# Optimization experiments

Hardware: AMD Instinct MI355X
Metric: run time of the kernel (lower is better)

## Reference

```python
import jax, jax.numpy as jnp
import numpy as np

B, N, H = 8, 512, 256
D2 = H // 2          # per-direction hidden = attention proj = 128
VOCAB, EMB = 100, 256
DIN0 = EMB + 3


def _sru_pp_layer(x, pad, Wq, Wk, Wv, Wu, vf, vr, bf, br):
    # x: (L, Bt, din); pad: (L, Bt) bool, True = padded position
    L, Bt, _ = x.shape
    d2 = Wu.shape[1] // 8
    q = x @ Wq                                   # (L,Bt,proj) attention projection
    k = q @ Wk
    v = q @ Wv
    scale = 1.0 / jnp.sqrt(jnp.asarray(q.shape[-1], q.dtype))
    scores = jnp.einsum('lbp,mbp->blm', q, k) * scale
    scores = jnp.where(pad.T[:, None, :], -1e9, scores)
    a = jnp.einsum('blm,mbp->lbp', jax.nn.softmax(scores, axis=-1), v) + q
    U = (a @ Wu).reshape(L, Bt, 2, 4, d2)        # 2 directions x 4 matrices

    def run_dir(Ud, padd, vf_d, vr_d, bf_d, br_d):
        def step(c, inp):
            u, p = inp                            # u: (Bt,4,d2), p: (Bt,)
            f = jax.nn.sigmoid(u[:, 1] + vf_d * c + bf_d)
            r = jax.nn.sigmoid(u[:, 2] + vr_d * c + br_d)
            c_new = f * c + (1.0 - f) * u[:, 0]
            c_new = jnp.where(p[:, None], c, c_new)
            h = jnp.where(p[:, None], 0.0, r * c_new + (1.0 - r) * u[:, 3])
            return c_new, h
        c0 = jnp.zeros((Bt, d2), x.dtype)
        _, hs = jax.lax.scan(step, c0, (Ud, padd))
        return hs

    hf = run_dir(U[:, :, 0], pad, vf[0], vr[0], bf[0], br[0])
    hb = run_dir(U[::-1, :, 1], pad[::-1], vf[1], vr[1], bf[1], br[1])[::-1]
    return jnp.concatenate([hf, hb], axis=-1)     # (L,Bt,2*d2)


def _forward(noisy_seqs, noisy_cords, mask, emb, params):
    Bb, Nn = noisy_seqs.shape
    X = noisy_cords[:, :, 1]                      # CA coordinates (B,N,3)
    m3 = mask[..., None]
    center = (X * m3).sum(1) / m3.sum(1)
    Xc = X - center[:, None] * m3
    C = jnp.einsum('bni,bnj->bij', Xc, Xc)        # (B,3,3) covariance
    _, V = jnp.linalg.eigh(jax.lax.stop_gradient(C))
    ops = jnp.asarray([[i, j, k] for i in (-1, 1) for j in (-1, 1) for k in (-1, 1)], X.dtype)
    F_ops = ops[None, :, None, :] * V[:, None]    # (B,8,3,3) sign-flipped frames
    hX = jnp.einsum('boji,bpj->bopi', F_ops, Xc).reshape(Bb * 8, Nn, 3)
    seq = jnp.where(noisy_seqs < 0, 82, noisy_seqs)
    hS = jnp.broadcast_to(emb[seq][:, None], (Bb, 8, Nn, emb.shape[1])).reshape(Bb * 8, Nn, -1)
    h = jnp.swapaxes(jnp.concatenate([hX, hS], -1), 0, 1)   # (N, B*8, EMB+3)
    pad = jnp.broadcast_to((mask == 0.0)[:, None], (Bb, 8, Nn)).reshape(Bb * 8, Nn).T
    for p in params:
        h = _sru_pp_layer(h, pad, *p)
    return jnp.swapaxes(h, 0, 1).reshape(Bb, 8, Nn, -1).mean(1)


def setup_inputs():
    key = jax.random.key(0)
    ks = [jax.random.fold_in(key, i) for i in range(32)]
    inp = {
        'noisy_seqs': jax.random.randint(ks[0], (B, N), 0, VOCAB, dtype=jnp.int32),
        'noisy_cords': jax.random.normal(ks[1], (B, N, 4, 3), jnp.float32),
        'mask': jnp.ones((B, N), jnp.float32),
        'emb': 0.02 * jax.random.normal(ks[2], (VOCAB, EMB), jnp.float32),
    }
    i = 3
    for l, din in enumerate([DIN0, H]):
        inp[f'Wq{l}'] = jax.random.normal(ks[i], (din, D2), jnp.float32) / np.sqrt(din); i += 1
        inp[f'Wk{l}'] = jax.random.normal(ks[i], (D2, D2), jnp.float32) / np.sqrt(D2); i += 1
        inp[f'Wv{l}'] = jax.random.normal(ks[i], (D2, D2), jnp.float32) / np.sqrt(D2); i += 1
        inp[f'Wu{l}'] = jax.random.normal(ks[i], (D2, 8 * D2), jnp.float32) / np.sqrt(D2); i += 1
        inp[f'vf{l}'] = 0.1 * jax.random.normal(ks[i], (2, D2), jnp.float32); i += 1
        inp[f'vr{l}'] = 0.1 * jax.random.normal(ks[i], (2, D2), jnp.float32); i += 1
        inp[f'bf{l}'] = jnp.zeros((2, D2), jnp.float32)
        inp[f'br{l}'] = jnp.zeros((2, D2), jnp.float32)
    return inp


def reference(noisy_seqs, noisy_cords, mask, emb,
              Wq0, Wk0, Wv0, Wu0, vf0, vr0, bf0, br0,
              Wq1, Wk1, Wv1, Wu1, vf1, vr1, bf1, br1):
    params = [(Wq0, Wk0, Wv0, Wu0, vf0, vr0, bf0, br0),
              (Wq1, Wk1, Wv1, Wu1, vf1, vr1, bf1, br1)]
    return _forward(noisy_seqs, noisy_cords, mask, emb, params)
```

## Files before the change

kernel.cpp:

```cpp
#include <hip/hip_runtime.h>
#include <hip/hip_bf16.h>
#include <math.h>

#define L_    512
#define F_    64
#define M_    (F_*L_)
#define D2_   128
#define H_    256
#define LOG2E_ 1.4426950408889634f

typedef unsigned short u16;
typedef __attribute__((ext_vector_type(8))) short s16x8;
typedef __attribute__((ext_vector_type(4))) float f32x4;

__device__ inline u16 bf_hi(float x) {
  union { float f; unsigned u; } v; v.f = x;
  unsigned r = v.u + 0x7fffu + ((v.u >> 16) & 1u);
  return (u16)(r >> 16);
}
__device__ inline float bf_to_f(u16 h) {
  union { float f; unsigned u; } v; v.u = ((unsigned)h) << 16; return v.f;
}
__device__ inline void split2(float x, u16& h, u16& l) {
  h = bf_hi(x);
  l = bf_hi(x - bf_to_f(h));
}
__device__ inline float exp2_fast(float x) {
#if __has_builtin(__builtin_amdgcn_exp2f)
  return __builtin_amdgcn_exp2f(x);
#else
  return __expf(x * 0.6931471805599453f);
#endif
}

#define RSPLIT_A 18432
#define RSPLIT_B 26624

__global__ void geom_kernel(const float* __restrict__ cords, const float* __restrict__ mask,
                            float* __restrict__ misc) {
  int b = blockIdx.x;
  int t = threadIdx.x;
  __shared__ float red[4][256];
  float sx=0.f, sy=0.f, sz=0.f, sm=0.f;
  for (int l = t; l < 512; l += 256) {
    float m = mask[b*512 + l];
    const float* X = cords + ((size_t)(b*512 + l)*4 + 1)*3;
    sx += X[0]*m; sy += X[1]*m; sz += X[2]*m; sm += m;
  }
  red[0][t]=sx; red[1][t]=sy; red[2][t]=sz; red[3][t]=sm;
  __syncthreads();
  for (int off=128; off>0; off>>=1) {
    if (t < off) { red[0][t]+=red[0][t+off]; red[1][t]+=red[1][t+off];
                   red[2][t]+=red[2][t+off]; red[3][t]+=red[3][t+off]; }
    __syncthreads();
  }
  float inv = 1.f/red[3][0];
  float cx = red[0][0]*inv, cy = red[1][0]*inv, cz = red[2][0]*inv;
  __syncthreads();
  __shared__ float red6[6][256];
  float c00=0,c01=0,c02=0,c11=0,c12=0,c22=0;
  for (int l = t; l < 512; l += 256) {
    float m = mask[b*512+l];
    const float* X = cords + ((size_t)(b*512+l)*4 + 1)*3;
    float x = X[0]-cx*m, y = X[1]-cy*m, z = X[2]-cz*m;
    c00+=x*x; c01+=x*y; c02+=x*z; c11+=y*y; c12+=y*z; c22+=z*z;
  }
  red6[0][t]=c00; red6[1][t]=c01; red6[2][t]=c02;
  red6[3][t]=c11; red6[4][t]=c12; red6[5][t]=c22;
  __syncthreads();
  for (int off=128; off>0; off>>=1) {
    if (t < off) for (int j=0;j<6;j++) red6[j][t]+=red6[j][t+off];
    __syncthreads();
  }
  if (t == 0) {
    double A[3][3], V[3][3];
    A[0][0]=red6[0][0]; A[0][1]=A[1][0]=red6[1][0]; A[0][2]=A[2][0]=red6[2][0];
    A[1][1]=red6[3][0]; A[1][2]=A[2][1]=red6[4][0]; A[2][2]=red6[5][0];
    for (int j=0;j<3;j++) for (int i=0;i<3;i++) V[j][i] = (i==j)?1.0:0.0;
    for (int sweep=0; sweep<10; ++sweep) {
      for (int p=0;p<2;p++) for (int q=p+1;q<3;q++) {
        double apq = A[p][q];
        if (fabs(apq) < 1e-18) continue;
        double app = A[p][p], aqq = A[q][q];
        double tau = (aqq - app) / (2.0*apq);
        double tt = (tau >= 0.0) ? 1.0/(tau + sqrt(1.0+tau*tau))
                                 : 1.0/(tau - sqrt(1.0+tau*tau));
        double cc = 1.0/sqrt(1.0+tt*tt), ss = tt*cc;
        A[p][p] = app - tt*apq;
        A[q][q] = aqq + tt*apq;
        A[p][q] = A[q][p] = 0.0;
        int r = 3 - p - q;
        double arp = A[r][p], arq = A[r][q];
        A[r][p] = A[p][r] = cc*arp - ss*arq;
        A[r][q] = A[q][r] = ss*arp + cc*arq;
        for (int rr2=0; rr2<3; ++rr2) {
          double vrp = V[rr2][p], vrq = V[rr2][q];
          V[rr2][p] = cc*vrp - ss*vrq;
          V[rr2][q] = ss*vrp + cc*vrq;
        }
      }
    }
    double w[3] = {A[0][0], A[1][1], A[2][2]};
    int idx[3] = {0,1,2};
    for (int i=0;i<2;i++) for (int j=0;j<2-i;j++)
      if (w[idx[j]] > w[idx[j+1]]) { int tmp=idx[j]; idx[j]=idx[j+1]; idx[j+1]=tmp; }
    for (int jj=0;jj<3;jj++) for (int ii=0;ii<3;ii++)
      misc[b*12 + jj*3 + ii] = (float)V[jj][idx[ii]];
    misc[b*12+9]=cx; misc[b*12+10]=cy; misc[b*12+11]=cz;
  }
}

__global__ void build_h0(const int* __restrict__ seqs, const float* __restrict__ cords,
                         const float* __restrict__ mask, const float* __restrict__ emb,
                         const float* __restrict__ misc,
                         u16* __restrict__ h0h, u16* __restrict__ h0l) {
  int t = threadIdx.x;
  int r = blockIdx.x*4 + (t >> 6);
  int lane = t & 63;
  int f = r >> 9, l = r & 511;
  int b = f >> 3, o = f & 7;
  u16* rh = h0h + (size_t)r * 288;
  u16* rl = h0l + (size_t)r * 288;
  if (lane == 0) {
    float m = mask[b*512 + l];
    const float* X = cords + ((size_t)(b*512 + l)*4 + 1)*3;
    const float* mb = misc + b*12;
    float x = X[0]-mb[9]*m, y = X[1]-mb[10]*m, z = X[2]-mb[11]*m;
    #pragma unroll
    for (int i=0;i<3;i++) {
      float sgn = ((o >> (2-i)) & 1) ? 1.f : -1.f;
      float val = sgn * (mb[0+i]*x + mb[3+i]*y + mb[6+i]*z);
      u16 h,lo; split2(val,h,lo); rh[i]=h; rl[i]=lo;
    }
  }
  if (lane < 29) { rh[259+lane] = 0; rl[259+lane] = 0; }
  int s = seqs[b*512 + l];
  if (s < 0) s = 82;
  const float4 e4 = *((const float4*)(emb + (size_t)s*256) + lane);
  float ev[4] = {e4.x, e4.y, e4.z, e4.w};
  #pragma unroll
  for (int i=0;i<4;i++) {
    u16 h,lo; split2(ev[i],h,lo);
    rh[3 + lane*4 + i] = h; rl[3 + lane*4 + i] = lo;
  }
}

__global__ void prep_w3(const float* __restrict__ Wq, const float* __restrict__ Wk,
                        const float* __restrict__ Wv,
                        u16* __restrict__ qTh, u16* __restrict__ qTl,
                        u16* __restrict__ kTh, u16* __restrict__ kTl,
                        u16* __restrict__ vTh, u16* __restrict__ vTl,
                        int Kq, int KPq) {
  int y = blockIdx.y;
  int n = blockIdx.x;
  const float* W = (y==0) ? Wq : (y==1) ? Wk : Wv;
  u16* Th = (y==0) ? qTh : (y==1) ? kTh : vTh;
  u16* Tl = (y==0) ? qTl : (y==1) ? kTl : vTl;
  const int K  = (y==0) ? Kq  : 128;
  const int KP = (y==0) ? KPq : 128;
  for (int k = threadIdx.x; k < KP; k += 128) {
    float x = (k < K) ? W[(size_t)k*128 + n] : 0.f;
    u16 h,l; split2(x,h,l);
    Th[(size_t)n*KP + k] = h; Tl[(size_t)n*KP + k] = l;
  }
}

__global__ void prep_wu(const float* __restrict__ Wu, u16* __restrict__ Th, u16* __restrict__ Tl) {
  int n = blockIdx.x;
  int dir = blockIdx.y;
  int k = threadIdx.x;
  int d = n >> 2, g = n & 3;
  float x = Wu[(size_t)k*1024 + (dir*4+g)*128 + d];
  if (g == 1 || g == 2) x *= LOG2E_;
  u16 h,l; split2(x,h,l);
  size_t o = ((size_t)dir*512 + n)*128 + k;
  Th[o]=h; Tl[o]=l;
}

template<int EPI>
__global__ __launch_bounds__(256) void gemm_bb(
    const u16* __restrict__ Ah, const u16* __restrict__ Al,
    const u16* __restrict__ Bh, const u16* __restrict__ Bl,
    int KP, int lda, int ldb,
    long aBatch, long bBatch, long cBatch,
    u16* __restrict__ Ch, u16* __restrict__ Cl, int ldc,
    float* __restrict__ Cf, float* __restrict__ CfB, float* __restrict__ CfC,
    const u16* __restrict__ rh, const u16* __restrict__ rl,
    const float* __restrict__ maskp, float scale)
{
  __shared__ u16 As[2][128][40];
  __shared__ u16 Bs[2][128][40];
  const int t = threadIdx.x;
  const int z = blockIdx.z;
  const int bm = blockIdx.x * 128, bn = blockIdx.y * 128;
  Ah += (size_t)z * aBatch; Al += (size_t)z * aBatch;
  Bh += (size_t)z * bBatch; Bl += (size_t)z * bBatch;

  const int lane = t & 63;
  const int w = t >> 6, wr = w >> 1, wc = w & 1;
  const int fr = lane & 15, g = lane >> 4;

  f32x4 acc[4][4] = {};

  for (int k0 = 0; k0 < KP; k0 += 32) {
    #pragma unroll
    for (int cc = 0; cc < 2; cc++) {
      int c = t + cc*256;
      int m = c >> 2, sub = c & 3;
      const size_t ga = (size_t)(bm + m)*lda + k0 + sub*8;
      const size_t gb = (size_t)(bn + m)*ldb + k0 + sub*8;
      *(int4*)&As[0][m][sub*8] = *(const int4*)(Ah + ga);
      *(int4*)&As[1][m][sub*8] = *(const int4*)(Al + ga);
      *(int4*)&Bs[0][m][sub*8] = *(const int4*)(Bh + gb);
      *(int4*)&Bs[1][m][sub*8] = *(const int4*)(Bl + gb);
    }
    __syncthreads();
    s16x8 af[4][2], bfr[4][2];
    #pragma unroll
    for (int i = 0; i < 4; i++) {
      af[i][0]  = *(const s16x8*)&As[0][wr*64 + i*16 + fr][g*8];
      af[i][1]  = *(const s16x8*)&As[1][wr*64 + i*16 + fr][g*8];
      bfr[i][0] = *(const s16x8*)&Bs[0][wc*64 + i*16 + fr][g*8];
      bfr[i][1] = *(const s16x8*)&Bs[1][wc*64 + i*16 + fr][g*8];
    }
    #pragma unroll
    for (int mi = 0; mi < 4; mi++)
      #pragma unroll
      for (int nj = 0; nj < 4; nj++)
        acc[mi][nj] = __builtin_amdgcn_mfma_f32_16x16x32_bf16(af[mi][0], bfr[nj][0], acc[mi][nj], 0,0,0);
    #pragma unroll
    for (int mi = 0; mi < 4; mi++)
      #pragma unroll
      for (int nj = 0; nj < 4; nj++)
        acc[mi][nj] = __builtin_amdgcn_mfma_f32_16x16x32_bf16(af[mi][0], bfr[nj][1], acc[mi][nj], 0,0,0);
    #pragma unroll
    for (int mi = 0; mi < 4; mi++)
      #pragma unroll
      for (int nj = 0; nj < 4; nj++)
        acc[mi][nj] = __builtin_amdgcn_mfma_f32_16x16x32_bf16(af[mi][1], bfr[nj][0], acc[mi][nj], 0,0,0);
    __syncthreads();
  }

  const int rbase = bm + wr*64, nbase = bn + wc*64;
  #pragma unroll
  for (int mi = 0; mi < 4; mi++) {
    #pragma unroll
    for (int nj = 0; nj < 4; nj++) {
      #pragma unroll
      for (int rg = 0; rg < 4; rg++) {
        int r = rbase + mi*16 + g*4 + rg;
        int n = nbase + nj*16 + fr;
        float val = acc[mi][nj][rg];
        if (EPI == 0) {
          size_t o = (size_t)r*ldc + n;
          u16 h,l; split2(val,h,l);
          Ch[o]=h; Cl[o]=l;
        } else if (EPI == 1) {
          size_t o = ((size_t)(r >> 9)*128 + n)*512 + (r & 511);
          u16 h,l; split2(val,h,l);
          Ch[o]=h; Cl[o]=l;
        } else if (EPI == 2) {
          float vv = val * scale;
          if (maskp[(z>>3)*512 + n] == 0.f) vv = -1e9f;
          Cf[(size_t)z*cBatch + (size_t)r*ldc + n] = vv;
        } else if (EPI == 3) {
          size_t o = (size_t)z*cBatch + (size_t)r*ldc + n;
          float vv = val + (bf_to_f(rh[o]) + bf_to_f(rl[o]));
          u16 h,l; split2(vv,h,l);
          Ch[o]=h; Cl[o]=l;
        } else {
          float* Up;
          if (r < RSPLIT_A)      Up = Cf  + (size_t)r*512;
          else if (r < RSPLIT_B) Up = CfB + (size_t)(r - RSPLIT_A)*512;
          else                   Up = CfC + (size_t)(r - RSPLIT_B)*512;
          Up[n] = val;
        }
      }
    }
  }
}

__global__ void softmax_split(float* __restrict__ S) {
  size_t row = blockIdx.x;
  float* p = S + row*512;
  u16* ph = (u16*)p;
  u16* pl = ph + 512;
  int t = threadIdx.x;
  float v[8];
  float mx = -1e30f;
  #pragma unroll
  for (int i=0;i<8;i++) { v[i] = p[t + i*64]; mx = fmaxf(mx, v[i]); }
  #pragma unroll
  for (int off=32; off>0; off>>=1) mx = fmaxf(mx, __shfl_xor(mx, off));
  float sum = 0.f;
  #pragma unroll
  for (int i=0;i<8;i++) { v[i] = __expf(v[i]-mx); sum += v[i]; }
  #pragma unroll
  for (int off=32; off>0; off>>=1) sum += __shfl_xor(sum, off);
  float invs = 1.f/sum;
  #pragma unroll
  for (int i=0;i<8;i++) {
    float x = v[i]*invs;
    u16 h,l; split2(x,h,l);
    ph[t + i*64] = h; pl[t + i*64] = l;
  }
}

#define CH_ 8
#define LOADC(buf, ch) do { \
  int _c = (ch); \
  _Pragma("unroll") \
  for (int s = 0; s < CH_; s++) { \
    int l = (_c*CH_ + s) ^ lxor; \
    buf[s] = *(const float4*)(Ubase + (size_t)l*512); \
  } \
  __builtin_amdgcn_sched_barrier(0); \
} while(0)

#define COMPC(buf, ch) do { \
  int _c = (ch); \
  float mk[CH_]; \
  _Pragma("unroll") \
  for (int s = 0; s < CH_; s++) { \
    int l = (_c*CH_ + s) ^ lxor; \
    mk[s] = msk[l]; \
  } \
  unsigned pk[CH_]; \
  _Pragma("unroll") \
  for (int s = 0; s < CH_; s++) { \
    float4 u = buf[s]; \
    float xf = (u.y + bfd) + vfd*cstate; \
    float xr = (u.z + brd) + vrd*cstate; \
    float fg = 1.f/(1.f + exp2_fast(-xf)); \
    float rg = 1.f/(1.f + exp2_fast(-xr)); \
    float cn = fg*(cstate - u.x) + u.x; \
    if (mk[s] == 0.f) cn = cstate; \
    float h = (mk[s] == 0.f) ? 0.f : (rg*(cn - u.w) + u.w); \
    cstate = cn; \
    u16 sh_, sl_; split2(h, sh_, sl_); \
    pk[s] = (unsigned)sh_ | ((unsigned)sl_ << 16); \
  } \
  __builtin_amdgcn_sched_barrier(0); \
  _Pragma("unroll") \
  for (int s = 0; s < CH_; s++) { \
    int l = (_c*CH_ + s) ^ lxor; \
    hpph[(size_t)l*256] = (u16)pk[s]; \
    hppl[(size_t)l*256] = (u16)(pk[s] >> 16); \
  } \
  __builtin_amdgcn_sched_barrier(0); \
} while(0)

__global__ __launch_bounds__(64, 1) void sru_scan(
                          const float* __restrict__ ua0, const float* __restrict__ ub0,
                          const float* __restrict__ uc0,
                          const float* __restrict__ ua1, const float* __restrict__ ub1,
                          const float* __restrict__ uc1,
                          const float* __restrict__ mask,
                          const float* __restrict__ vf, const float* __restrict__ vr,
                          const float* __restrict__ bf, const float* __restrict__ br,
                          u16* __restrict__ hph, u16* __restrict__ hpl,
                          int dirArg) {
  const int blk = blockIdx.x;
  const int f = blk >> 1;
  const int hh = blk & 1;
  const int dir = dirArg + blockIdx.y;
  const int t = threadIdx.x;
  const int b = f >> 3;
  __shared__ float msk[512];
  for (int i = t; i < 512; i += 64) msk[i] = mask[b*512 + i];
  __syncthreads();
  const int lxor = dir ? 511 : 0;
  const int d = hh*64 + t;
  const float vfd = vf[dir*128 + d]*LOG2E_, vrd = vr[dir*128 + d]*LOG2E_;
  const float bfd = bf[dir*128 + d]*LOG2E_, brd = br[dir*128 + d]*LOG2E_;
  const size_t fbase = (size_t)f * 512;
  const float* ua = dir ? ua1 : ua0;
  const float* ub = dir ? ub1 : ub0;
  const float* uc = dir ? uc1 : uc0;
  const float* Uf;
  if (f < 36)      Uf = ua + (size_t)f*(512*512);
  else if (f < 52) Uf = ub + (size_t)(f-36)*(512*512);
  else             Uf = uc + (size_t)(f-52)*(512*512);
  const float* Ubase = Uf + d*4;
  u16* hpph = hph + fbase*256 + (size_t)dir*128 + d;
  u16* hppl = hpl + fbase*256 + (size_t)dir*128 + d;

  float4 b0[CH_], b1[CH_], b2[CH_], b3[CH_];
  LOADC(b0, 0); LOADC(b1, 1);
  float cstate = 0.f;
  #pragma unroll 1
  for (int q4 = 0; q4 < 15; q4++) {
    const int base = q4*4;
    LOADC(b2, base+2);
    COMPC(b0, base);
    LOADC(b3, base+3);
    COMPC(b1, base+1);
    LOADC(b0, base+4);
    COMPC(b2, base+2);
    LOADC(b1, base+5);
    COMPC(b3, base+3);
  }
  LOADC(b2, 62);
  COMPC(b0, 60);
  LOADC(b3, 63);
  COMPC(b1, 61);
  COMPC(b2, 62);
  COMPC(b3, 63);
}

__global__ void mean_kernel(const u16* __restrict__ hph, const u16* __restrict__ hpl,
                            float* __restrict__ out) {
  int i = blockIdx.x*256 + threadIdx.x;
  int row = i >> 5;
  int c8  = i & 31;
  int b = row >> 9, l = row & 511;
  float acc[8] = {};
  #pragma unroll
  for (int o=0;o<8;o++) {
    size_t off = ((size_t)((b*8+o)*512 + l))*256 + c8*8;
    union { int4 v; u16 s[8]; } hv, lv;
    hv.v = *(const int4*)(hph + off);
    lv.v = *(const int4*)(hpl + off);
    #pragma unroll
    for (int j=0;j<8;j++)
      acc[j] += bf_to_f(hv.s[j]) + bf_to_f(lv.s[j]);
  }
  float4 q0, q1;
  q0.x=acc[0]*0.125f; q0.y=acc[1]*0.125f; q0.z=acc[2]*0.125f; q0.w=acc[3]*0.125f;
  q1.x=acc[4]*0.125f; q1.y=acc[5]*0.125f; q1.z=acc[6]*0.125f; q1.w=acc[7]*0.125f;
  float* op = out + (size_t)row*256 + c8*8;
  *(float4*)op = q0;
  *(float4*)(op+4) = q1;
}

extern "C" void kernel_launch(void* const* d_in, const int* in_sizes, int n_in,
                              void* d_out, int out_size, void* d_ws, size_t ws_size,
                              hipStream_t stream) {
  const int*   seqs  = (const int*)d_in[0];
  const float* cords = (const float*)d_in[1];
  const float* mask  = (const float*)d_in[2];
  const float* emb   = (const float*)d_in[3];
  const float* Wq[2] = {(const float*)d_in[4],  (const float*)d_in[12]};
  const float* Wk[2] = {(const float*)d_in[5],  (const float*)d_in[13]};
  const float* Wv[2] = {(const float*)d_in[6],  (const float*)d_in[14]};
  const float* Wu[2] = {(const float*)d_in[7],  (const float*)d_in[15]};
  const float* vf[2] = {(const float*)d_in[8],  (const float*)d_in[16]};
  const float* vr[2] = {(const float*)d_in[9],  (const float*)d_in[17]};
  const float* bfp[2]= {(const float*)d_in[10], (const float*)d_in[18]};
  const float* brp[2]= {(const float*)d_in[11], (const float*)d_in[19]};

  const size_t H0_B = 2*(size_t)M_*288*2;
  const size_t Q_B  = 2*(size_t)M_*128*2;
  const size_t S_B  = (size_t)M_*512*4;
  const size_t HP_B = 2*(size_t)M_*256*2;
  const size_t W_B  = (2*128*288 + 4*128*128 + 2*1024*128)*2;

  const size_t NEED_MERGED = 4096 + H0_B + 3*Q_B + S_B + HP_B + W_B;
  const bool merged = (ws_size >= NEED_MERGED);

  char* base = (char*)d_ws;
  float* misc = (float*)base;
  u16* h0p_h = (u16*)(base + 4096);
  u16* h0p_l = h0p_h + (size_t)M_*288;
  u16* q_h   = (u16*)(base + 4096 + H0_B);
  u16* q_l   = q_h + (size_t)M_*128;
  u16* k_h   = (u16*)(base + 4096 + H0_B + Q_B);
  u16* k_l   = k_h + (size_t)M_*128;
  u16* a_h = k_h;  u16* a_l = k_l;

  u16 *vT_h, *vT_l;
  float *S, *hp_end_w;
  u16 *hp_h, *hp_l;
  float *U1A, *U1B, *U1C;
  if (merged) {
    vT_h = (u16*)(base + 4096 + H0_B + 2*Q_B);
    vT_l = vT_h + (size_t)M_*128;
    S    = (float*)(base + 4096 + H0_B + 3*Q_B);
    hp_h = (u16*)((char*)S + S_B);
    hp_l = hp_h + (size_t)M_*256;
    hp_end_w = (float*)((char*)hp_h + HP_B);
    U1A = (float*)h0p_h;
    U1B = (float*)q_h;
    U1C = (float*)vT_h;
  } else {
    S    = (float*)(base + 4096 + H0_B + 2*Q_B);
    hp_h = (u16*)((char*)S + S_B);
    hp_l = hp_h + (size_t)M_*256;
    vT_h = hp_h; vT_l = hp_l;
    hp_end_w = (float*)((char*)hp_h + HP_B);
    U1A = S; U1B = S + (size_t)RSPLIT_A*512; U1C = S + (size_t)RSPLIT_B*512;
  }
  float* U0A = S;
  float* U0B = S + (size_t)RSPLIT_A*512;
  float* U0C = S + (size_t)RSPLIT_B*512;

  u16* wqT_h = (u16*)hp_end_w;
  u16* wqT_l = wqT_h + 128*288;
  u16* wkT_h = wqT_l + 128*288;
  u16* wkT_l = wkT_h + 128*128;
  u16* wvT_h = wkT_l + 128*128;
  u16* wvT_l = wvT_h + 128*128;
  u16* wuT_h = wvT_l + 128*128;
  u16* wuT_l = wuT_h + 1024*128;

  geom_kernel<<<8, 256, 0, stream>>>(cords, mask, misc);
  build_h0<<<M_/4, 256, 0, stream>>>(seqs, cords, mask, emb, misc, h0p_h, h0p_l);

  const float scale = 0.08838834764831845f;
  for (int layer = 0; layer < 2; ++layer) {
    const u16* Ah_in = layer ? hp_h : h0p_h;
    const u16* Al_in = layer ? hp_l : h0p_l;
    const int  Kq    = layer ? 256 : 259;
    const int  KPq   = layer ? 256 : 288;

    prep_w3<<<dim3(128,3), 128, 0, stream>>>(Wq[layer], Wk[layer], Wv[layer],
        wqT_h, wqT_l, wkT_h, wkT_l, wvT_h, wvT_l, Kq, KPq);
    prep_wu<<<dim3(512,2), 128, 0, stream>>>(Wu[layer], wuT_h, wuT_l);

    gemm_bb<0><<<dim3(256,1,1), 256, 0, stream>>>(Ah_in, Al_in, wqT_h, wqT_l,
        KPq, KPq, KPq, 0,0,0, q_h, q_l, 128, nullptr,nullptr,nullptr, nullptr,nullptr, nullptr, 0.f);
    gemm_bb<0><<<dim3(256,1,1), 256, 0, stream>>>(q_h, q_l, wkT_h, wkT_l,
        128, 128, 128, 0,0,0, k_h, k_l, 128, nullptr,nullptr,nullptr, nullptr,nullptr, nullptr, 0.f);
    gemm_bb<1><<<dim3(256,1,1), 256, 0, stream>>>(q_h, q_l, wvT_h, wvT_l,
        128, 128, 128, 0,0,0, vT_h, vT_l, 0, nullptr,nullptr,nullptr, nullptr,nullptr, nullptr, 0.f);
    gemm_bb<2><<<dim3(4,4,64), 256, 0, stream>>>(q_h, q_l, k_h, k_l,
        128, 128, 128, 512*128, 512*128, 512*512, nullptr,nullptr, 512, S,nullptr,nullptr,
        nullptr,nullptr, mask, scale);
    softmax_split<<<M_, 64, 0, stream>>>(S);
    gemm_bb<3><<<dim3(4,1,64), 256, 0, stream>>>((const u16*)S, (const u16*)S + 512, vT_h, vT_l,
        512, 1024, 512, 512*1024, 128*512, 512*128, a_h, a_l, 128, nullptr,nullptr,nullptr,
        q_h, q_l, nullptr, 0.f);

    gemm_bb<4><<<dim3(256,4,1), 256, 0, stream>>>(a_h, a_l,
        wuT_h, wuT_l, 128, 128, 128, 0,0,0, nullptr,nullptr, 512,
        U0A, U0B, U0C, nullptr,nullptr, nullptr, 0.f);
    if (merged) {
      gemm_bb<4><<<dim3(256,4,1), 256, 0, stream>>>(a_h, a_l,
          wuT_h + (size_t)512*128, wuT_l + (size_t)512*128, 128, 128, 128, 0,0,0,
          nullptr,nullptr, 512, U1A, U1B, U1C, nullptr,nullptr, nullptr, 0.f);
      sru_scan<<<dim3(128,2), 64, 0, stream>>>(U0A,U0B,U0C, U1A,U1B,U1C, mask,
          vf[layer], vr[layer], bfp[layer], brp[layer], hp_h, hp_l, 0);
    } else {
      sru_scan<<<dim3(128,1), 64, 0, stream>>>(U0A,U0B,U0C, U0A,U0B,U0C, mask,
          vf[layer], vr[layer], bfp[layer], brp[layer], hp_h, hp_l, 0);
      gemm_bb<4><<<dim3(256,4,1), 256, 0, stream>>>(a_h, a_l,
          wuT_h + (size_t)512*128, wuT_l + (size_t)512*128, 128, 128, 128, 0,0,0,
          nullptr,nullptr, 512, U0A, U0B, U0C, nullptr,nullptr, nullptr, 0.f);
      sru_scan<<<dim3(128,1), 64, 0, stream>>>(U0A,U0B,U0C, U0A,U0B,U0C, mask,
          vf[layer], vr[layer], bfp[layer], brp[layer], hp_h, hp_l, 1);
    }
  }
  mean_kernel<<<512, 256, 0, stream>>>(hp_h, hp_l, (float*)d_out);
}
```

Measured before the change: 539.0 us.

## Precompose Wq·Wk/Wq·Wv, fuse QKV GEMM, move bias and mask into U epilogue

Precomputes Wq@Wk and Wq@Wv on device so q, k and v come from one combined GEMM launch that reads the input once, instead of three chained GEMMs. The U projection epilogue now folds in the negated log2e bias and encodes padding as saturating gate values, so the scan no longer loads the mask or does selects, and it uses rcp/exp2 intrinsics. Both directions' U GEMMs are merged into one launch. The last layer writes fp32 h directly so the mean kernel reads floats instead of hi/lo bf16 pairs. Precomposing the weights changes the rounding path, and the saturating-gate mask trick depends on exp2 overflow behaving as intended.

```diff
diff --git a/kernel.cpp b/kernel.cpp
--- a/kernel.cpp
+++ b/kernel.cpp
@@ -30,6 +30,13 @@
   return __builtin_amdgcn_exp2f(x);
 #else
   return __expf(x * 0.6931471805599453f);
+#endif
+}
+__device__ inline float rcp_fast(float x) {
+#if __has_builtin(__builtin_amdgcn_rcpf)
+  return __builtin_amdgcn_rcpf(x);
+#else
+  return 1.f/x;
 #endif
 }
 
@@ -145,36 +152,52 @@
   }
 }
 
-__global__ void prep_w3(const float* __restrict__ Wq, const float* __restrict__ Wk,
-                        const float* __restrict__ Wv,
-                        u16* __restrict__ qTh, u16* __restrict__ qTl,
-                        u16* __restrict__ kTh, u16* __restrict__ kTl,
-                        u16* __restrict__ vTh, u16* __restrict__ vTl,
-                        int Kq, int KPq) {
+__global__ void prep_wqkv_mul(const float* __restrict__ Wq, const float* __restrict__ Wk,
+                              const float* __restrict__ Wv,
+                              float* __restrict__ wqk, float* __restrict__ wqv) {
+  int k = blockIdx.x;
+  int y = blockIdx.y;
+  int t = threadIdx.x;
+  __shared__ float row[128];
+  row[t] = Wq[(size_t)k*128 + t];
+  __syncthreads();
+  const float* W2 = y ? Wv : Wk;
+  float acc = 0.f;
+  for (int j = 0; j < 128; j++) acc += row[j] * W2[(size_t)j*128 + t];
+  (y ? wqv : wqk)[(size_t)k*128 + t] = acc;
+}
+
+__global__ void prep_wT3(const float* __restrict__ Wq, const float* __restrict__ wqk,
+                         const float* __restrict__ wqv,
+                         u16* __restrict__ Th, u16* __restrict__ Tl,
+                         int K, int KP) {
   int y = blockIdx.y;
   int n = blockIdx.x;
-  const float* W = (y==0) ? Wq : (y==1) ? Wk : Wv;
-  u16* Th = (y==0) ? qTh : (y==1) ? kTh : vTh;
-  u16* Tl = (y==0) ? qTl : (y==1) ? kTl : vTl;
-  const int K  = (y==0) ? Kq  : 128;
-  const int KP = (y==0) ? KPq : 128;
+  const float* W = (y==0) ? Wq : (y==1) ? wqk : wqv;
+  int row = y*128 + n;
   for (int k = threadIdx.x; k < KP; k += 128) {
     float x = (k < K) ? W[(size_t)k*128 + n] : 0.f;
     u16 h,l; split2(x,h,l);
-    Th[(size_t)n*KP + k] = h; Tl[(size_t)n*KP + k] = l;
-  }
-}
-
-__global__ void prep_wu(const float* __restrict__ Wu, u16* __restrict__ Th, u16* __restrict__ Tl) {
+    Th[(size_t)row*KP + k] = h; Tl[(size_t)row*KP + k] = l;
+  }
+}
+
+__global__ void prep_wu(const float* __restrict__ Wu, u16* __restrict__ Th, u16* __restrict__ Tl,
+                        const float* __restrict__ bfv, const float* __restrict__ brv,
+                        float* __restrict__ nbf, float* __restrict__ nbr) {
   int n = blockIdx.x;
   int dir = blockIdx.y;
   int k = threadIdx.x;
   int d = n >> 2, g = n & 3;
   float x = Wu[(size_t)k*1024 + (dir*4+g)*128 + d];
-  if (g == 1 || g == 2) x *= LOG2E_;
+  if (g == 1 || g == 2) x *= -LOG2E_;
   u16 h,l; split2(x,h,l);
   size_t o = ((size_t)dir*512 + n)*128 + k;
   Th[o]=h; Tl[o]=l;
+  if (n == 0) {
+    nbf[dir*128 + k] = bfv[dir*128 + k] * (-LOG2E_);
+    nbr[dir*128 + k] = brv[dir*128 + k] * (-LOG2E_);
+  }
 }
 
 template<int EPI>
@@ -184,9 +207,13 @@
     int KP, int lda, int ldb,
     long aBatch, long bBatch, long cBatch,
     u16* __restrict__ Ch, u16* __restrict__ Cl, int ldc,
-    float* __restrict__ Cf, float* __restrict__ CfB, float* __restrict__ CfC,
+    u16* __restrict__ Dh, u16* __restrict__ Dl,
+    u16* __restrict__ Eh, u16* __restrict__ El,
+    float* __restrict__ F0, float* __restrict__ F1, float* __restrict__ F2,
+    float* __restrict__ F3, float* __restrict__ F4, float* __restrict__ F5,
     const u16* __restrict__ rh, const u16* __restrict__ rl,
-    const float* __restrict__ maskp, float scale)
+    const float* __restrict__ maskp, const float* __restrict__ nbf,
+    const float* __restrict__ nbr, float scale, int dirOff)
 {
   __shared__ u16 As[2][128][40];
   __shared__ u16 Bs[2][128][40];
@@ -242,6 +269,16 @@
   }
 
   const int rbase = bm + wr*64, nbase = bn + wc*64;
+
+  const bool isD1 = (bn >= 512);
+  const int dirU = dirOff + (isD1 ? 1 : 0);
+  const float* nbfd = (EPI==4) ? nbf + dirU*128 : nullptr;
+  const float* nbrd = (EPI==4) ? nbr + dirU*128 : nullptr;
+  float* tA = isD1 ? F3 : F0;
+  float* tB = isD1 ? F4 : F1;
+  float* tC = isD1 ? F5 : F2;
+  const int gg = fr & 3;
+
   #pragma unroll
   for (int mi = 0; mi < 4; mi++) {
     #pragma unroll
@@ -251,29 +288,41 @@
         int r = rbase + mi*16 + g*4 + rg;
         int n = nbase + nj*16 + fr;
         float val = acc[mi][nj][rg];
-        if (EPI == 0) {
-          size_t o = (size_t)r*ldc + n;
-          u16 h,l; split2(val,h,l);
-          Ch[o]=h; Cl[o]=l;
-        } else if (EPI == 1) {
-          size_t o = ((size_t)(r >> 9)*128 + n)*512 + (r & 511);
-          u16 h,l; split2(val,h,l);
-          Ch[o]=h; Cl[o]=l;
-        } else if (EPI == 2) {
+        if (EPI == 2) {
           float vv = val * scale;
           if (maskp[(z>>3)*512 + n] == 0.f) vv = -1e9f;
-          Cf[(size_t)z*cBatch + (size_t)r*ldc + n] = vv;
+          F0[(size_t)z*cBatch + (size_t)r*ldc + n] = vv;
         } else if (EPI == 3) {
           size_t o = (size_t)z*cBatch + (size_t)r*ldc + n;
           float vv = val + (bf_to_f(rh[o]) + bf_to_f(rl[o]));
           u16 h,l; split2(vv,h,l);
           Ch[o]=h; Cl[o]=l;
+        } else if (EPI == 4) {
+          int nloc = (n & 511);
+          int dd = nloc >> 2;
+          float bfv2 = nbfd[dd], brv2 = nbrd[dd];
+          float addv = (gg==1) ? bfv2 : (gg==2) ? brv2 : 0.f;
+          val += addv;
+          float mv = maskp[(r>>12)*512 + (r & 511)];
+          float ovr = (gg==1) ? -16384.f : (gg==2) ? 16384.f : (gg==3) ? 0.f : val;
+          val = (mv == 0.f) ? ovr : val;
+          float* Up;
+          if (r < RSPLIT_A)      Up = tA + (size_t)r*512;
+          else if (r < RSPLIT_B) Up = tB + (size_t)(r - RSPLIT_A)*512;
+          else                   Up = tC + (size_t)(r - RSPLIT_B)*512;
+          Up[nloc] = val;
         } else {
-          float* Up;
-          if (r < RSPLIT_A)      Up = Cf  + (size_t)r*512;
-          else if (r < RSPLIT_B) Up = CfB + (size_t)(r - RSPLIT_A)*512;
-          else                   Up = CfC + (size_t)(r - RSPLIT_B)*512;
-          Up[n] = val;
+          u16 h,l; split2(val,h,l);
+          if (blockIdx.y == 0) {
+            size_t o = (size_t)r*128 + n;
+            Ch[o]=h; Cl[o]=l;
+          } else if (blockIdx.y == 1) {
+            size_t o = (size_t)r*128 + (n - 128);
+            Dh[o]=h; Dl[o]=l;
+          } else {
+            size_t o = ((size_t)(r >> 9)*128 + (n - 256))*512 + (r & 511);
+            Eh[o]=h; El[o]=l;
+          }
         }
       }
     }
@@ -319,60 +368,46 @@
 
 #define COMPC(buf, ch) do { \
   int _c = (ch); \
-  float mk[CH_]; \
   _Pragma("unroll") \
   for (int s = 0; s < CH_; s++) { \
     int l = (_c*CH_ + s) ^ lxor; \
-    mk[s] = msk[l]; \
-  } \
-  unsigned pk[CH_]; \
-  _Pragma("unroll") \
-  for (int s = 0; s < CH_; s++) { \
     float4 u = buf[s]; \
-    float xf = (u.y + bfd) + vfd*cstate; \
-    float xr = (u.z + brd) + vrd*cstate; \
-    float fg = 1.f/(1.f + exp2_fast(-xf)); \
-    float rg = 1.f/(1.f + exp2_fast(-xr)); \
-    float cn = fg*(cstate - u.x) + u.x; \
-    if (mk[s] == 0.f) cn = cstate; \
-    float h = (mk[s] == 0.f) ? 0.f : (rg*(cn - u.w) + u.w); \
+    float ef = exp2_fast(fmaf(nvfd, cstate, u.y)); \
+    float fg = rcp_fast(1.f + ef); \
+    float er = exp2_fast(fmaf(nvrd, cstate, u.z)); \
+    float rg = rcp_fast(1.f + er); \
+    float cn = fmaf(fg, cstate - u.x, u.x); \
+    float h  = fmaf(rg, cn - u.w, u.w); \
     cstate = cn; \
-    u16 sh_, sl_; split2(h, sh_, sl_); \
-    pk[s] = (unsigned)sh_ | ((unsigned)sl_ << 16); \
-  } \
-  __builtin_amdgcn_sched_barrier(0); \
-  _Pragma("unroll") \
-  for (int s = 0; s < CH_; s++) { \
-    int l = (_c*CH_ + s) ^ lxor; \
-    hpph[(size_t)l*256] = (u16)pk[s]; \
-    hppl[(size_t)l*256] = (u16)(pk[s] >> 16); \
+    if (PAIRS) { \
+      u16 sh_, sl_; split2(h, sh_, sl_); \
+      hpph[(size_t)l*256] = sh_; \
+      hppl[(size_t)l*256] = sl_; \
+    } else { \
+      h32p[(size_t)l*256] = h; \
+    } \
   } \
   __builtin_amdgcn_sched_barrier(0); \
 } while(0)
 
+template<int PAIRS>
 __global__ __launch_bounds__(64, 1) void sru_scan(
                           const float* __restrict__ ua0, const float* __restrict__ ub0,
                           const float* __restrict__ uc0,
                           const float* __restrict__ ua1, const float* __restrict__ ub1,
                           const float* __restrict__ uc1,
-                          const float* __restrict__ mask,
                           const float* __restrict__ vf, const float* __restrict__ vr,
-                          const float* __restrict__ bf, const float* __restrict__ br,
                           u16* __restrict__ hph, u16* __restrict__ hpl,
-                          int dirArg) {
+                          float* __restrict__ h32, int dirArg) {
   const int blk = blockIdx.x;
   const int f = blk >> 1;
   const int hh = blk & 1;
   const int dir = dirArg + blockIdx.y;
   const int t = threadIdx.x;
-  const int b = f >> 3;
-  __shared__ float msk[512];
-  for (int i = t; i < 512; i += 64) msk[i] = mask[b*512 + i];
-  __syncthreads();
   const int lxor = dir ? 511 : 0;
   const int d = hh*64 + t;
-  const float vfd = vf[dir*128 + d]*LOG2E_, vrd = vr[dir*128 + d]*LOG2E_;
-  const float bfd = bf[dir*128 + d]*LOG2E_, brd = br[dir*128 + d]*LOG2E_;
+  const float nvfd = vf[dir*128 + d] * (-LOG2E_);
+  const float nvrd = vr[dir*128 + d] * (-LOG2E_);
   const size_t fbase = (size_t)f * 512;
   const float* ua = dir ? ua1 : ua0;
   const float* ub = dir ? ub1 : ub0;
@@ -384,6 +419,7 @@
   const float* Ubase = Uf + d*4;
   u16* hpph = hph + fbase*256 + (size_t)dir*128 + d;
   u16* hppl = hpl + fbase*256 + (size_t)dir*128 + d;
+  float* h32p = h32 + fbase*256 + (size_t)dir*128 + d;
 
   float4 b0[CH_], b1[CH_], b2[CH_], b3[CH_];
   LOADC(b0, 0); LOADC(b1, 1);
@@ -408,29 +444,20 @@
   COMPC(b3, 63);
 }
 
-__global__ void mean_kernel(const u16* __restrict__ hph, const u16* __restrict__ hpl,
-                            float* __restrict__ out) {
+__global__ void mean_kernel(const float* __restrict__ h2, float* __restrict__ out) {
   int i = blockIdx.x*256 + threadIdx.x;
-  int row = i >> 5;
-  int c8  = i & 31;
+  int row = i >> 6;
+  int c4  = i & 63;
   int b = row >> 9, l = row & 511;
-  float acc[8] = {};
+  float ax=0.f, ay=0.f, az=0.f, aw=0.f;
   #pragma unroll
   for (int o=0;o<8;o++) {
-    size_t off = ((size_t)((b*8+o)*512 + l))*256 + c8*8;
-    union { int4 v; u16 s[8]; } hv, lv;
-    hv.v = *(const int4*)(hph + off);
-    lv.v = *(const int4*)(hpl + off);
-    #pragma unroll
-    for (int j=0;j<8;j++)
-      acc[j] += bf_to_f(hv.s[j]) + bf_to_f(lv.s[j]);
-  }
-  float4 q0, q1;
-  q0.x=acc[0]*0.125f; q0.y=acc[1]*0.125f; q0.z=acc[2]*0.125f; q0.w=acc[3]*0.125f;
-  q1.x=acc[4]*0.125f; q1.y=acc[5]*0.125f; q1.z=acc[6]*0.125f; q1.w=acc[7]*0.125f;
-  float* op = out + (size_t)row*256 + c8*8;
-  *(float4*)op = q0;
-  *(float4*)(op+4) = q1;
+    const float4* p = (const float4*)(h2 + ((size_t)((b*8+o)*512 + l))*256) + c4;
+    float4 e = *p;
+    ax += e.x; ay += e.y; az += e.z; aw += e.w;
+  }
+  float4 r; r.x = ax*0.125f; r.y = ay*0.125f; r.z = az*0.125f; r.w = aw*0.125f;
+  ((float4*)out)[i] = r;
 }
 
 extern "C" void kernel_launch(void* const* d_in, const int* in_sizes, int n_in,
@@ -453,7 +480,7 @@
   const size_t Q_B  = 2*(size_t)M_*128*2;
   const size_t S_B  = (size_t)M_*512*4;
   const size_t HP_B = 2*(size_t)M_*256*2;
-  const size_t W_B  = (2*128*288 + 4*128*128 + 2*1024*128)*2;
+  const size_t W_B  = (size_t)(2*1024*128)*2 + 2*256*4;
 
   const size_t NEED_MERGED = 4096 + H0_B + 3*Q_B + S_B + HP_B + W_B;
   const bool merged = (ws_size >= NEED_MERGED);
@@ -469,7 +496,7 @@
   u16* a_h = k_h;  u16* a_l = k_l;
 
   u16 *vT_h, *vT_l;
-  float *S, *hp_end_w;
+  float *S, *tail_w;
   u16 *hp_h, *hp_l;
   float *U1A, *U1B, *U1C;
   if (merged) {
@@ -478,7 +505,7 @@
     S    = (float*)(base + 4096 + H0_B + 3*Q_B);
     hp_h = (u16*)((char*)S + S_B);
     hp_l = hp_h + (size_t)M_*256;
-    hp_end_w = (float*)((char*)hp_h + HP_B);
+    tail_w = (float*)((char*)hp_h + HP_B);
     U1A = (float*)h0p_h;
     U1B = (float*)q_h;
     U1C = (float*)vT_h;
@@ -487,21 +514,22 @@
     hp_h = (u16*)((char*)S + S_B);
     hp_l = hp_h + (size_t)M_*256;
     vT_h = hp_h; vT_l = hp_l;
-    hp_end_w = (float*)((char*)hp_h + HP_B);
+    tail_w = (float*)((char*)hp_h + HP_B);
     U1A = S; U1B = S + (size_t)RSPLIT_A*512; U1C = S + (size_t)RSPLIT_B*512;
   }
   float* U0A = S;
   float* U0B = S + (size_t)RSPLIT_A*512;
   float* U0C = S + (size_t)RSPLIT_B*512;
-
-  u16* wqT_h = (u16*)hp_end_w;
-  u16* wqT_l = wqT_h + 128*288;
-  u16* wkT_h = wqT_l + 128*288;
-  u16* wkT_l = wkT_h + 128*128;
-  u16* wvT_h = wkT_l + 128*128;
-  u16* wvT_l = wvT_h + 128*128;
-  u16* wuT_h = wvT_l + 128*128;
+  float* h32 = (float*)hp_h;
+
+  float* wqk32 = S;
+  float* wqv32 = wqk32 + 288*128;
+  u16*   wT3h  = (u16*)(wqv32 + 288*128);
+  u16*   wT3l  = wT3h + 384*288;
+  u16* wuT_h = (u16*)tail_w;
   u16* wuT_l = wuT_h + 1024*128;
+  float* nbf = (float*)(wuT_l + 1024*128);
+  float* nbr = nbf + 256;
 
   geom_kernel<<<8, 256, 0, stream>>>(cords, mask, misc);
   build_h0<<<M_/4, 256, 0, stream>>>(seqs, cords, mask, emb, misc, h0p_h, h0p_l);
@@ -513,42 +541,54 @@
     const int  Kq    = layer ? 256 : 259;
     const int  KPq   = layer ? 256 : 288;
 
-    prep_w3<<<dim3(128,3), 128, 0, stream>>>(Wq[layer], Wk[layer], Wv[layer],
-        wqT_h, wqT_l, wkT_h, wkT_l, wvT_h, wvT_l, Kq, KPq);
-    prep_wu<<<dim3(512,2), 128, 0, stream>>>(Wu[layer], wuT_h, wuT_l);
-
-    gemm_bb<0><<<dim3(256,1,1), 256, 0, stream>>>(Ah_in, Al_in, wqT_h, wqT_l,
-        KPq, KPq, KPq, 0,0,0, q_h, q_l, 128, nullptr,nullptr,nullptr, nullptr,nullptr, nullptr, 0.f);
-    gemm_bb<0><<<dim3(256,1,1), 256, 0, stream>>>(q_h, q_l, wkT_h, wkT_l,
-        128, 128, 128, 0,0,0, k_h, k_l, 128, nullptr,nullptr,nullptr, nullptr,nullptr, nullptr, 0.f);
-    gemm_bb<1><<<dim3(256,1,1), 256, 0, stream>>>(q_h, q_l, wvT_h, wvT_l,
-        128, 128, 128, 0,0,0, vT_h, vT_l, 0, nullptr,nullptr,nullptr, nullptr,nullptr, nullptr, 0.f);
+    prep_wqkv_mul<<<dim3(Kq,2), 128, 0, stream>>>(Wq[layer], Wk[layer], Wv[layer], wqk32, wqv32);
+    prep_wT3<<<dim3(128,3), 128, 0, stream>>>(Wq[layer], wqk32, wqv32, wT3h, wT3l, Kq, KPq);
+    prep_wu<<<dim3(512,2), 128, 0, stream>>>(Wu[layer], wuT_h, wuT_l, bfp[layer], brp[layer], nbf, nbr);
+
+    gemm_bb<5><<<dim3(256,3,1), 256, 0, stream>>>(Ah_in, Al_in, wT3h, wT3l,
+        KPq, KPq, KPq, 0,0,0, q_h, q_l, 128, k_h, k_l, vT_h, vT_l,
+        nullptr,nullptr,nullptr,nullptr,nullptr,nullptr,
+        nullptr,nullptr, nullptr,nullptr,nullptr, 0.f, 0);
     gemm_bb<2><<<dim3(4,4,64), 256, 0, stream>>>(q_h, q_l, k_h, k_l,
-        128, 128, 128, 512*128, 512*128, 512*512, nullptr,nullptr, 512, S,nullptr,nullptr,
-        nullptr,nullptr, mask, scale);
+        128, 128, 128, 512*128, 512*128, 512*512, nullptr,nullptr, 512,
+        nullptr,nullptr,nullptr,nullptr,
+        S,nullptr,nullptr,nullptr,nullptr,nullptr,
+        nullptr,nullptr, mask,nullptr,nullptr, scale, 0);
     softmax_split<<<M_, 64, 0, stream>>>(S);
     gemm_bb<3><<<dim3(4,1,64), 256, 0, stream>>>((const u16*)S, (const u16*)S + 512, vT_h, vT_l,
-        512, 1024, 512, 512*1024, 128*512, 512*128, a_h, a_l, 128, nullptr,nullptr,nullptr,
-        q_h, q_l, nullptr, 0.f);
-
-    gemm_bb<4><<<dim3(256,4,1), 256, 0, stream>>>(a_h, a_l,
-        wuT_h, wuT_l, 128, 128, 128, 0,0,0, nullptr,nullptr, 512,
-        U0A, U0B, U0C, nullptr,nullptr, nullptr, 0.f);
+        512, 1024, 512, 512*1024, 128*512, 512*128, a_h, a_l, 128,
+        nullptr,nullptr,nullptr,nullptr,
+        nullptr,nullptr,nullptr,nullptr,nullptr,nullptr,
+        q_h, q_l, nullptr,nullptr,nullptr, 0.f, 0);
+
     if (merged) {
-      gemm_bb<4><<<dim3(256,4,1), 256, 0, stream>>>(a_h, a_l,
-          wuT_h + (size_t)512*128, wuT_l + (size_t)512*128, 128, 128, 128, 0,0,0,
-          nullptr,nullptr, 512, U1A, U1B, U1C, nullptr,nullptr, nullptr, 0.f);
-      sru_scan<<<dim3(128,2), 64, 0, stream>>>(U0A,U0B,U0C, U1A,U1B,U1C, mask,
-          vf[layer], vr[layer], bfp[layer], brp[layer], hp_h, hp_l, 0);
+      gemm_bb<4><<<dim3(256,8,1), 256, 0, stream>>>(a_h, a_l, wuT_h, wuT_l,
+          128, 128, 128, 0,0,0, nullptr,nullptr, 512,
+          nullptr,nullptr,nullptr,nullptr,
+          U0A,U0B,U0C, U1A,U1B,U1C,
+          nullptr,nullptr, mask, nbf, nbr, 0.f, 0);
+      if (layer == 0)
+        sru_scan<1><<<dim3(128,2), 64, 0, stream>>>(U0A,U0B,U0C, U1A,U1B,U1C,
+            vf[layer], vr[layer], hp_h, hp_l, h32, 0);
+      else
+        sru_scan<0><<<dim3(128,2), 64, 0, stream>>>(U0A,U0B,U0C, U1A,U1B,U1C,
+            vf[layer], vr[layer], hp_h, hp_l, h32, 0);
     } else {
-      sru_scan<<<dim3(128,1), 64, 0, stream>>>(U0A,U0B,U0C, U0A,U0B,U0C, mask,
-          vf[layer], vr[layer], bfp[layer], brp[layer], hp_h, hp_l, 0);
-      gemm_bb<4><<<dim3(256,4,1), 256, 0, stream>>>(a_h, a_l,
-          wuT_h + (size_t)512*128, wuT_l + (size_t)512*128, 128, 128, 128, 0,0,0,
-          nullptr,nullptr, 512, U0A, U0B, U0C, nullptr,nullptr, nullptr, 0.f);
-      sru_scan<<<dim3(128,1), 64, 0, stream>>>(U0A,U0B,U0C, U0A,U0B,U0C, mask,
-          vf[layer], vr[layer], bfp[layer], brp[layer], hp_h, hp_l, 1);
+      for (int dir = 0; dir < 2; ++dir) {
+        gemm_bb<4><<<dim3(256,4,1), 256, 0, stream>>>(a_h, a_l,
+            wuT_h + (size_t)dir*512*128, wuT_l + (size_t)dir*512*128,
+            128, 128, 128, 0,0,0, nullptr,nullptr, 512,
+            nullptr,nullptr,nullptr,nullptr,
+            U0A,U0B,U0C, U0A,U0B,U0C,
+            nullptr,nullptr, mask, nbf, nbr, 0.f, dir);
+        if (layer == 0)
+          sru_scan<1><<<dim3(128,1), 64, 0, stream>>>(U0A,U0B,U0C, U0A,U0B,U0C,
+              vf[layer], vr[layer], hp_h, hp_l, h32, dir);
+        else
+          sru_scan<0><<<dim3(128,1), 64, 0, stream>>>(U0A,U0B,U0C, U0A,U0B,U0C,
+              vf[layer], vr[layer], hp_h, hp_l, h32, dir);
+      }
     }
   }
-  mean_kernel<<<512, 256, 0, stream>>>(hp_h, hp_l, (float*)d_out);
-}
+  mean_kernel<<<1024, 256, 0, stream>>>(h32, (float*)d_out);
+}
```

Measured after the change: 587.4 us. 1.09x slower.
